# Performance work log

Hardware: AMD Instinct MI355X
Metric: run time of the kernel (lower is better)

## Reference

```python
import jax, jax.numpy as jnp
import numpy as np

B, S, D, F, E = 4, 2048, 1024, 4096, 8


def setup_inputs() -> dict:
    key = jax.random.key(0)
    ks = jax.random.split(key, 7)
    s1 = 1.0 / np.sqrt(D)
    s2 = 1.0 / np.sqrt(F)
    x = jax.random.normal(ks[0], (B, S, D), dtype=jnp.float32)
    # Stacked expert weights: linear1 (D->F), linear2 (F->D), torch default uniform init
    W1 = jax.random.uniform(ks[1], (E, D, F), jnp.float32, -s1, s1)
    b1 = jax.random.uniform(ks[2], (E, F), jnp.float32, -s1, s1)
    W2 = jax.random.uniform(ks[3], (E, F, D), jnp.float32, -s2, s2)
    b2 = jax.random.uniform(ks[4], (E, D), jnp.float32, -s2, s2)
    Wr = jax.random.uniform(ks[5], (D, E), jnp.float32, -s1, s1)
    br = jax.random.uniform(ks[6], (E,), jnp.float32, -s1, s1)
    return {"x": x, "W1": W1, "b1": b1, "W2": W2, "b2": b2, "Wr": Wr, "br": br}


def reference(x, W1, b1, W2, b2, Wr, br):
    b, s, d = x.shape
    e = Wr.shape[1]
    logits = x @ Wr + br                      # [B,S,E]
    idx = jnp.argmax(logits, axis=-1)         # top-1 expert per token
    probs = jax.nn.softmax(logits, axis=-1)
    gates = jnp.take_along_axis(probs, idx[..., None], axis=-1)[..., 0]  # [B,S]
    xf = x.reshape(-1, d)                     # [N,D]
    idxf = idx.reshape(-1)
    gf = gates.reshape(-1)
    out = jnp.zeros_like(xf)
    for ei in range(e):                       # fixed small expert count
        h = jax.nn.gelu(xf @ W1[ei] + b1[ei], approximate=False)  # exact gelu like F.gelu
        y = h @ W2[ei] + b2[ei]
        mask = (idxf == ei).astype(xf.dtype)
        out = out + y * (gf * mask)[:, None]
    return out.reshape(b, s, d)
```

## Files before the change

kernel.cpp:

```cpp
#include <hip/hip_runtime.h>
#include <stdint.h>
#include <math.h>

#define NTOK 8192
#define DIM  1024
#define FDIM 4096
#define NEXP 8

typedef __bf16 bf16x8 __attribute__((ext_vector_type(8)));
typedef float floatx4 __attribute__((ext_vector_type(4)));
typedef unsigned int u32;

__device__ __forceinline__ unsigned short f2b(float f) {
  union { float f; unsigned u; } v; v.f = f;
  return (unsigned short)((v.u + 0x7fffu + ((v.u >> 16) & 1u)) >> 16);
}

__device__ __forceinline__ float gelu_f(float x) {
  float u = 1.5957691216f * x * (1.0f + 0.044715f * x * x);
  return x / (1.0f + __expf(-u));
}

__device__ __forceinline__ void async_cp16(const unsigned short* g, unsigned short* l) {
  __builtin_amdgcn_global_load_lds((__attribute__((address_space(1))) u32*)g,
                                   (__attribute__((address_space(3))) u32*)l, 16, 0, 0);
}

__global__ __launch_bounds__(256) void router_k(
    const float* __restrict__ x, const float* __restrict__ Wr,
    const float* __restrict__ br, int* __restrict__ idx,
    float* __restrict__ gate, int* __restrict__ ctrl) {
  int t = (int)((blockIdx.x * 256 + threadIdx.x) >> 6);
  int lane = threadIdx.x & 63;
  const float* xr = x + (size_t)t * DIM;
  float acc[NEXP];
#pragma unroll
  for (int e = 0; e < NEXP; e++) acc[e] = 0.f;
#pragma unroll
  for (int k = 0; k < DIM / 64; k++) {
    int d = k * 64 + lane;
    float xv = xr[d];
    const float4* wp = (const float4*)(Wr + (size_t)d * NEXP);
    float4 w0 = wp[0], w1 = wp[1];
    acc[0] += xv * w0.x; acc[1] += xv * w0.y;
    acc[2] += xv * w0.z; acc[3] += xv * w0.w;
    acc[4] += xv * w1.x; acc[5] += xv * w1.y;
    acc[6] += xv * w1.z; acc[7] += xv * w1.w;
  }
#pragma unroll
  for (int off = 32; off > 0; off >>= 1) {
#pragma unroll
    for (int e = 0; e < NEXP; e++) acc[e] += __shfl_xor(acc[e], off, 64);
  }
  if (lane == 0) {
    float mx = -3.4e38f; int best = 0;
#pragma unroll
    for (int e = 0; e < NEXP; e++) {
      float l = acc[e] + br[e];
      if (l > mx) { mx = l; best = e; }
    }
    float s = 0.f;
#pragma unroll
    for (int e = 0; e < NEXP; e++) s += expf(acc[e] + br[e] - mx);
    idx[t] = best;
    gate[t] = 1.f / s;
    atomicAdd(&ctrl[best], 1);
  }
}

__global__ void scan_k(int* __restrict__ ctrl) {
  int off = 0, ts = 0;
  ctrl[8] = 0; ctrl[25] = 0;
  for (int e = 0; e < NEXP; e++) {
    off += ctrl[e];                 ctrl[9 + e]  = off;
    ts  += (ctrl[e] + 127) >> 7;    ctrl[26 + e] = ts;
  }
}

__global__ __launch_bounds__(256) void scatter_k(
    const float* __restrict__ x, const int* __restrict__ idx,
    const float* __restrict__ gate, int* __restrict__ ctrl,
    unsigned short* __restrict__ Xb, int* __restrict__ token_dst,
    float* __restrict__ gate_p) {
  __shared__ int s_pos;
  int t = blockIdx.x;
  if (threadIdx.x == 0) {
    int e = idx[t];
    s_pos = ctrl[8 + e] + atomicAdd(&ctrl[17 + e], 1);
  }
  __syncthreads();
  int pos = s_pos;
  if (threadIdx.x == 0) { token_dst[pos] = t; gate_p[pos] = gate[t]; }
  float4 v = ((const float4*)(x + (size_t)t * DIM))[threadIdx.x];
  ushort4 o;
  o.x = f2b(v.x); o.y = f2b(v.y); o.z = f2b(v.z); o.w = f2b(v.w);
  ((ushort4*)(Xb + (size_t)pos * DIM))[threadIdx.x] = o;
}

__global__ __launch_bounds__(256) void transpose_cvt_k(
    const float* __restrict__ in, unsigned short* __restrict__ out,
    int R, int C) {
  __shared__ float tile[64][65];
  __shared__ unsigned short obuf[64][72];
  size_t base = (size_t)blockIdx.z * (size_t)R * (size_t)C;
  int c0 = blockIdx.x * 64, r0 = blockIdx.y * 64;
  int t = threadIdx.x;
  int rr = t >> 4, cc = (t & 15) * 4;
#pragma unroll
  for (int k = 0; k < 64; k += 16) {
    float4 v = *(const float4*)&in[base + (size_t)(r0 + rr + k) * C + c0 + cc];
    tile[rr + k][cc] = v.x; tile[rr + k][cc + 1] = v.y;
    tile[rr + k][cc + 2] = v.z; tile[rr + k][cc + 3] = v.w;
  }
  __syncthreads();
  int cr = t >> 4, rb = (t & 15) * 4;
#pragma unroll
  for (int k = 0; k < 64; k += 16) {
    ushort4 o;
    o.x = f2b(tile[rb + 0][cr + k]); o.y = f2b(tile[rb + 1][cr + k]);
    o.z = f2b(tile[rb + 2][cr + k]); o.w = f2b(tile[rb + 3][cr + k]);
    *(ushort4*)&obuf[cr + k][rb] = o;
  }
  __syncthreads();
  int r2 = t >> 3, c8 = (t & 7) * 8;
#pragma unroll
  for (int k = 0; k < 64; k += 32)
    *(uint4*)&out[base + (size_t)(c0 + r2 + k) * R + r0 + c8] = *(const uint4*)&obuf[r2 + k][c8];
}

__global__ __launch_bounds__(256) void gemm1_k(
    const unsigned short* __restrict__ Amat, const unsigned short* __restrict__ Bmat,
    const float* __restrict__ bias, unsigned short* __restrict__ Hout,
    const int* __restrict__ ctrl) {
  __shared__ unsigned short lds[16384];
  unsigned short* A_lds = lds;
  unsigned short* B_lds = lds + 8192;

  int mt = blockIdx.y;
  if (mt >= ctrl[33]) return;
  int e = 0;
  while (e < 7 && ctrl[26 + e] <= mt) e++;
  int mt_local = mt - ctrl[25 + e];
  int m0 = ctrl[8 + e] + mt_local * 128;
  int cnt = ctrl[e] - mt_local * 128; if (cnt > 128) cnt = 128;
  int c0 = blockIdx.x * 128;
  const unsigned short* B = Bmat + (size_t)e * FDIM * DIM;

  int tid = threadIdx.x;
  int lane = tid & 63, wave = tid >> 6;
  int wr = wave >> 1, wc = wave & 1;
  int grp = lane >> 4, m16 = lane & 15;

  int lr = lane >> 3;
  int cchunk = (lane & 7) ^ lr;
  const unsigned short* srcA[4];
  const unsigned short* srcB[4];
  unsigned short* dstA[4];
  unsigned short* dstB[4];
#pragma unroll
  for (int q = 0; q < 4; q++) {
    int brow = wave * 32 + q * 8;
    int arow = m0 + brow + lr; if (arow > NTOK - 1) arow = NTOK - 1;
    srcA[q] = Amat + (size_t)arow * DIM + cchunk * 8;
    srcB[q] = B + (size_t)(c0 + brow + lr) * DIM + cchunk * 8;
    dstA[q] = A_lds + brow * 64;
    dstB[q] = B_lds + brow * 64;
  }

  floatx4 acc[4][4];
  floatx4 zero = {0.f, 0.f, 0.f, 0.f};
#pragma unroll
  for (int i = 0; i < 4; i++)
#pragma unroll
    for (int j = 0; j < 4; j++) acc[i][j] = zero;

  int x7 = m16 & 7;
  int rowA[4], rowB[4];
#pragma unroll
  for (int i = 0; i < 4; i++) {
    rowA[i] = (wr * 64 + i * 16 + m16) * 64;
    rowB[i] = (wc * 64 + i * 16 + m16) * 64;
  }

  for (int kk = 0; kk < DIM; kk += 64) {
#pragma unroll
    for (int q = 0; q < 4; q++) async_cp16(srcA[q], dstA[q]);
#pragma unroll
    for (int q = 0; q < 4; q++) async_cp16(srcB[q], dstB[q]);
#pragma unroll
    for (int q = 0; q < 4; q++) { srcA[q] += 64; srcB[q] += 64; }
    __syncthreads();
    bf16x8 af[2][4], bfr[2][4];
#pragma unroll
    for (int h = 0; h < 2; h++) {
      int off = (((h << 2) | grp) ^ x7) << 3;
#pragma unroll
      for (int i = 0; i < 4; i++) {
        af[h][i]  = *(const bf16x8*)&A_lds[rowA[i] + off];
        bfr[h][i] = *(const bf16x8*)&B_lds[rowB[i] + off];
      }
    }
#pragma unroll
    for (int h = 0; h < 2; h++)
#pragma unroll
      for (int i = 0; i < 4; i++)
#pragma unroll
        for (int j = 0; j < 4; j++)
          acc[i][j] = __builtin_amdgcn_mfma_f32_16x16x32_bf16(af[h][i], bfr[h][j], acc[i][j], 0, 0, 0);
    __syncthreads();
  }

  float bs[4];
#pragma unroll
  for (int j = 0; j < 4; j++) bs[j] = bias[(size_t)e * FDIM + c0 + wc * 64 + j * 16 + m16];

  unsigned short* st = lds + wave * 4096;
#pragma unroll
  for (int i = 0; i < 4; i++)
#pragma unroll
    for (int j = 0; j < 4; j++)
#pragma unroll
      for (int r = 0; r < 4; r++)
        st[(i * 16 + grp * 4 + r) * 64 + j * 16 + m16] = f2b(gelu_f(acc[i][j][r] + bs[j]));
  __syncthreads();
  int lr8 = lane >> 3, c8 = (lane & 7) * 8;
  int colb = c0 + wc * 64 + c8;
#pragma unroll
  for (int rr = 0; rr < 8; rr++) {
    int row = rr * 8 + lr8;
    int gm = wr * 64 + row;
    if (gm < cnt)
      *(uint4*)&Hout[(size_t)(m0 + gm) * FDIM + colb] = *(const uint4*)&st[row * 64 + c8];
  }
}

__global__ __launch_bounds__(256) void gemm2_k(
    const unsigned short* __restrict__ Hmat, const unsigned short* __restrict__ W2b,
    float* __restrict__ P, const int* __restrict__ ctrl) {
  __shared__ unsigned short lds[16384];
  unsigned short* A_lds = lds;
  unsigned short* B_lds = lds + 8192;

  int mt = blockIdx.y;
  if (mt >= ctrl[33]) return;
  int e = 0;
  while (e < 7 && ctrl[26 + e] <= mt) e++;
  int mt_local = mt - ctrl[25 + e];
  int m0 = ctrl[8 + e] + mt_local * 128;
  int cnt = ctrl[e] - mt_local * 128; if (cnt > 128) cnt = 128;
  int c0 = blockIdx.x * 128;
  int chunk = blockIdx.z;
  int k0 = chunk * (FDIM / 2);
  const unsigned short* B = W2b + (size_t)e * DIM * FDIM + k0;
  const unsigned short* A = Hmat + k0;
  float* Pc = P + (size_t)chunk * NTOK * DIM;

  int tid = threadIdx.x;
  int lane = tid & 63, wave = tid >> 6;
  int wr = wave >> 1, wc = wave & 1;
  int grp = lane >> 4, m16 = lane & 15;

  int lr = lane >> 3;
  int cchunk = (lane & 7) ^ lr;
  const unsigned short* srcA[4];
  const unsigned short* srcB[4];
  unsigned short* dstA[4];
  unsigned short* dstB[4];
#pragma unroll
  for (int q = 0; q < 4; q++) {
    int brow = wave * 32 + q * 8;
    int arow = m0 + brow + lr; if (arow > NTOK - 1) arow = NTOK - 1;
    srcA[q] = A + (size_t)arow * FDIM + cchunk * 8;
    srcB[q] = B + (size_t)(c0 + brow + lr) * FDIM + cchunk * 8;
    dstA[q] = A_lds + brow * 64;
    dstB[q] = B_lds + brow * 64;
  }

  floatx4 acc[4][4];
  floatx4 zero = {0.f, 0.f, 0.f, 0.f};
#pragma unroll
  for (int i = 0; i < 4; i++)
#pragma unroll
    for (int j = 0; j < 4; j++) acc[i][j] = zero;

  int x7 = m16 & 7;
  int rowA[4], rowB[4];
#pragma unroll
  for (int i = 0; i < 4; i++) {
    rowA[i] = (wr * 64 + i * 16 + m16) * 64;
    rowB[i] = (wc * 64 + i * 16 + m16) * 64;
  }

  for (int kk = 0; kk < FDIM / 2; kk += 64) {
#pragma unroll
    for (int q = 0; q < 4; q++) async_cp16(srcA[q], dstA[q]);
#pragma unroll
    for (int q = 0; q < 4; q++) async_cp16(srcB[q], dstB[q]);
#pragma unroll
    for (int q = 0; q < 4; q++) { srcA[q] += 64; srcB[q] += 64; }
    __syncthreads();
    bf16x8 af[2][4], bfr[2][4];
#pragma unroll
    for (int h = 0; h < 2; h++) {
      int off = (((h << 2) | grp) ^ x7) << 3;
#pragma unroll
      for (int i = 0; i < 4; i++) {
        af[h][i]  = *(const bf16x8*)&A_lds[rowA[i] + off];
        bfr[h][i] = *(const bf16x8*)&B_lds[rowB[i] + off];
      }
    }
#pragma unroll
    for (int h = 0; h < 2; h++)
#pragma unroll
      for (int i = 0; i < 4; i++)
#pragma unroll
        for (int j = 0; j < 4; j++)
          acc[i][j] = __builtin_amdgcn_mfma_f32_16x16x32_bf16(af[h][i], bfr[h][j], acc[i][j], 0, 0, 0);
    __syncthreads();
  }

#pragma unroll
  for (int i = 0; i < 4; i++) {
    int rb = wr * 64 + i * 16 + grp * 4;
#pragma unroll
    for (int r = 0; r < 4; r++) {
      int lm = rb + r;
      if (lm < cnt) {
#pragma unroll
        for (int j = 0; j < 4; j++) {
          int col = c0 + wc * 64 + j * 16 + m16;
          Pc[(size_t)(m0 + lm) * DIM + col] = acc[i][j][r];
        }
      }
    }
  }
}

__global__ __launch_bounds__(256) void reduce_k(
    const float* __restrict__ P, const float* __restrict__ b2,
    float* __restrict__ out, const int* __restrict__ token_dst,
    const float* __restrict__ gate_p, const int* __restrict__ ctrl) {
  int row = blockIdx.x;
  int e = 0;
  while (e < 7 && ctrl[9 + e] <= row) e++;
  int t = token_dst[row];
  float g = gate_p[row];
  int c = threadIdx.x * 4;
  float4 p0 = *(const float4*)&P[(size_t)row * DIM + c];
  float4 p1 = *(const float4*)&P[(size_t)(NTOK + row) * DIM + c];
  float4 bb = *(const float4*)&b2[(size_t)e * DIM + c];
  float4 o;
  o.x = (p0.x + p1.x + bb.x) * g;
  o.y = (p0.y + p1.y + bb.y) * g;
  o.z = (p0.z + p1.z + bb.z) * g;
  o.w = (p0.w + p1.w + bb.w) * g;
  *(float4*)&out[(size_t)t * DIM + c] = o;
}

extern "C" void kernel_launch(void* const* d_in, const int* in_sizes, int n_in,
                              void* d_out, int out_size, void* d_ws, size_t ws_size,
                              hipStream_t stream) {
  const float* x  = (const float*)d_in[0];
  const float* W1 = (const float*)d_in[1];
  const float* b1 = (const float*)d_in[2];
  const float* W2 = (const float*)d_in[3];
  const float* b2 = (const float*)d_in[4];
  const float* Wr = (const float*)d_in[5];
  const float* br = (const float*)d_in[6];
  float* out = (float*)d_out;

  char* w = (char*)d_ws;
  int*   ctrl      = (int*)w;
  int*   idx       = (int*)(w + 1024);
  float* gate      = (float*)(w + 1024 + 4 * NTOK);
  int*   token_dst = (int*)(w + 1024 + 8 * NTOK);
  float* gate_p    = (float*)(w + 1024 + 12 * NTOK);
  unsigned short* Xb  = (unsigned short*)(w + (1ull << 18));
  unsigned short* H   = (unsigned short*)(w + (20ull << 20));
  unsigned short* W1b = (unsigned short*)(w + (88ull << 20));
  unsigned short* W2b = (unsigned short*)(w + (156ull << 20));
  float*          P   = (float*)(w + (88ull << 20));

  hipMemsetAsync(ctrl, 0, 256, stream);
  router_k<<<NTOK / 4, 256, 0, stream>>>(x, Wr, br, idx, gate, ctrl);
  scan_k<<<1, 1, 0, stream>>>(ctrl);
  scatter_k<<<NTOK, 256, 0, stream>>>(x, idx, gate, ctrl, Xb, token_dst, gate_p);
  transpose_cvt_k<<<dim3(FDIM / 64, DIM / 64, NEXP), 256, 0, stream>>>(W1, W1b, DIM, FDIM);
  transpose_cvt_k<<<dim3(DIM / 64, FDIM / 64, NEXP), 256, 0, stream>>>(W2, W2b, FDIM, DIM);
  gemm1_k<<<dim3(FDIM / 128, 72), 256, 0, stream>>>(Xb, W1b, b1, H, ctrl);
  gemm2_k<<<dim3(DIM / 128, 72, 2), 256, 0, stream>>>(H, W2b, P, ctrl);
  reduce_k<<<NTOK, 256, 0, stream>>>(P, b2, out, token_dst, gate_p, ctrl);
}
```

Before: 792.1 us.

## Fuse bias/gate epilogue into gemm2, drop split-K, merge weight transposes, pad LDS

Removes the split-K partial buffer and the separate reduce kernel: gemm2 now runs the full K range and applies the bias and gate, scattering results directly to output rows. The two weight transpose/convert launches are merged into a single launch. The gemm1 epilogue staging buffer gets a padded row stride to reduce LDS bank conflicts. The trade-off is that gemm2 has half as many blocks, each with a K loop twice as long, which lowers parallelism, and its output stores are scattered by token.

```diff
diff --git a/kernel.cpp b/kernel.cpp
--- a/kernel.cpp
+++ b/kernel.cpp
@@ -97,18 +97,27 @@
   ((ushort4*)(Xb + (size_t)pos * DIM))[threadIdx.x] = o;
 }
 
-__global__ __launch_bounds__(256) void transpose_cvt_k(
-    const float* __restrict__ in, unsigned short* __restrict__ out,
-    int R, int C) {
+__global__ __launch_bounds__(256) void transpose_cvt2_k(
+    const float* __restrict__ W1, unsigned short* __restrict__ W1b,
+    const float* __restrict__ W2, unsigned short* __restrict__ W2b) {
   __shared__ float tile[64][65];
   __shared__ unsigned short obuf[64][72];
-  size_t base = (size_t)blockIdx.z * (size_t)R * (size_t)C;
-  int c0 = blockIdx.x * 64, r0 = blockIdx.y * 64;
+  int z = blockIdx.z;
+  const float* in; unsigned short* out; int R, C, tc, tr;
+  if (z < NEXP) {
+    in = W1 + (size_t)z * DIM * FDIM; out = W1b + (size_t)z * DIM * FDIM;
+    R = DIM; C = FDIM; tc = blockIdx.x; tr = blockIdx.y;
+  } else {
+    int e = z - NEXP;
+    in = W2 + (size_t)e * FDIM * DIM; out = W2b + (size_t)e * FDIM * DIM;
+    R = FDIM; C = DIM; tc = blockIdx.y; tr = blockIdx.x;
+  }
+  int c0 = tc * 64, r0 = tr * 64;
   int t = threadIdx.x;
   int rr = t >> 4, cc = (t & 15) * 4;
 #pragma unroll
   for (int k = 0; k < 64; k += 16) {
-    float4 v = *(const float4*)&in[base + (size_t)(r0 + rr + k) * C + c0 + cc];
+    float4 v = *(const float4*)&in[(size_t)(r0 + rr + k) * C + c0 + cc];
     tile[rr + k][cc] = v.x; tile[rr + k][cc + 1] = v.y;
     tile[rr + k][cc + 2] = v.z; tile[rr + k][cc + 3] = v.w;
   }
@@ -125,14 +134,14 @@
   int r2 = t >> 3, c8 = (t & 7) * 8;
 #pragma unroll
   for (int k = 0; k < 64; k += 32)
-    *(uint4*)&out[base + (size_t)(c0 + r2 + k) * R + r0 + c8] = *(const uint4*)&obuf[r2 + k][c8];
+    *(uint4*)&out[(size_t)(c0 + r2 + k) * R + r0 + c8] = *(const uint4*)&obuf[r2 + k][c8];
 }
 
 __global__ __launch_bounds__(256) void gemm1_k(
     const unsigned short* __restrict__ Amat, const unsigned short* __restrict__ Bmat,
     const float* __restrict__ bias, unsigned short* __restrict__ Hout,
     const int* __restrict__ ctrl) {
-  __shared__ unsigned short lds[16384];
+  __shared__ unsigned short lds[17408];
   unsigned short* A_lds = lds;
   unsigned short* B_lds = lds + 8192;
 
@@ -214,14 +223,14 @@
 #pragma unroll
   for (int j = 0; j < 4; j++) bs[j] = bias[(size_t)e * FDIM + c0 + wc * 64 + j * 16 + m16];
 
-  unsigned short* st = lds + wave * 4096;
+  unsigned short* st = lds + wave * 4352;
 #pragma unroll
   for (int i = 0; i < 4; i++)
 #pragma unroll
     for (int j = 0; j < 4; j++)
 #pragma unroll
       for (int r = 0; r < 4; r++)
-        st[(i * 16 + grp * 4 + r) * 64 + j * 16 + m16] = f2b(gelu_f(acc[i][j][r] + bs[j]));
+        st[(i * 16 + grp * 4 + r) * 68 + j * 16 + m16] = f2b(gelu_f(acc[i][j][r] + bs[j]));
   __syncthreads();
   int lr8 = lane >> 3, c8 = (lane & 7) * 8;
   int colb = c0 + wc * 64 + c8;
@@ -229,14 +238,20 @@
   for (int rr = 0; rr < 8; rr++) {
     int row = rr * 8 + lr8;
     int gm = wr * 64 + row;
-    if (gm < cnt)
-      *(uint4*)&Hout[(size_t)(m0 + gm) * FDIM + colb] = *(const uint4*)&st[row * 64 + c8];
+    if (gm < cnt) {
+      uint2 a = *(const uint2*)&st[row * 68 + c8];
+      uint2 b = *(const uint2*)&st[row * 68 + c8 + 4];
+      uint4 v; v.x = a.x; v.y = a.y; v.z = b.x; v.w = b.y;
+      *(uint4*)&Hout[(size_t)(m0 + gm) * FDIM + colb] = v;
+    }
   }
 }
 
 __global__ __launch_bounds__(256) void gemm2_k(
     const unsigned short* __restrict__ Hmat, const unsigned short* __restrict__ W2b,
-    float* __restrict__ P, const int* __restrict__ ctrl) {
+    const float* __restrict__ b2, float* __restrict__ out,
+    const int* __restrict__ token_dst, const float* __restrict__ gate_p,
+    const int* __restrict__ ctrl) {
   __shared__ unsigned short lds[16384];
   unsigned short* A_lds = lds;
   unsigned short* B_lds = lds + 8192;
@@ -249,11 +264,7 @@
   int m0 = ctrl[8 + e] + mt_local * 128;
   int cnt = ctrl[e] - mt_local * 128; if (cnt > 128) cnt = 128;
   int c0 = blockIdx.x * 128;
-  int chunk = blockIdx.z;
-  int k0 = chunk * (FDIM / 2);
-  const unsigned short* B = W2b + (size_t)e * DIM * FDIM + k0;
-  const unsigned short* A = Hmat + k0;
-  float* Pc = P + (size_t)chunk * NTOK * DIM;
+  const unsigned short* B = W2b + (size_t)e * DIM * FDIM;
 
   int tid = threadIdx.x;
   int lane = tid & 63, wave = tid >> 6;
@@ -270,7 +281,7 @@
   for (int q = 0; q < 4; q++) {
     int brow = wave * 32 + q * 8;
     int arow = m0 + brow + lr; if (arow > NTOK - 1) arow = NTOK - 1;
-    srcA[q] = A + (size_t)arow * FDIM + cchunk * 8;
+    srcA[q] = Hmat + (size_t)arow * FDIM + cchunk * 8;
     srcB[q] = B + (size_t)(c0 + brow + lr) * FDIM + cchunk * 8;
     dstA[q] = A_lds + brow * 64;
     dstB[q] = B_lds + brow * 64;
@@ -291,7 +302,7 @@
     rowB[i] = (wc * 64 + i * 16 + m16) * 64;
   }
 
-  for (int kk = 0; kk < FDIM / 2; kk += 64) {
+  for (int kk = 0; kk < FDIM; kk += 64) {
 #pragma unroll
     for (int q = 0; q < 4; q++) async_cp16(srcA[q], dstA[q]);
 #pragma unroll
@@ -319,6 +330,10 @@
     __syncthreads();
   }
 
+  float bs[4];
+#pragma unroll
+  for (int j = 0; j < 4; j++) bs[j] = b2[(size_t)e * DIM + c0 + wc * 64 + j * 16 + m16];
+
 #pragma unroll
   for (int i = 0; i < 4; i++) {
     int rb = wr * 64 + i * 16 + grp * 4;
@@ -326,35 +341,16 @@
     for (int r = 0; r < 4; r++) {
       int lm = rb + r;
       if (lm < cnt) {
+        int t = token_dst[m0 + lm];
+        float g = gate_p[m0 + lm];
 #pragma unroll
         for (int j = 0; j < 4; j++) {
           int col = c0 + wc * 64 + j * 16 + m16;
-          Pc[(size_t)(m0 + lm) * DIM + col] = acc[i][j][r];
+          out[(size_t)t * DIM + col] = (acc[i][j][r] + bs[j]) * g;
         }
       }
     }
   }
-}
-
-__global__ __launch_bounds__(256) void reduce_k(
-    const float* __restrict__ P, const float* __restrict__ b2,
-    float* __restrict__ out, const int* __restrict__ token_dst,
-    const float* __restrict__ gate_p, const int* __restrict__ ctrl) {
-  int row = blockIdx.x;
-  int e = 0;
-  while (e < 7 && ctrl[9 + e] <= row) e++;
-  int t = token_dst[row];
-  float g = gate_p[row];
-  int c = threadIdx.x * 4;
-  float4 p0 = *(const float4*)&P[(size_t)row * DIM + c];
-  float4 p1 = *(const float4*)&P[(size_t)(NTOK + row) * DIM + c];
-  float4 bb = *(const float4*)&b2[(size_t)e * DIM + c];
-  float4 o;
-  o.x = (p0.x + p1.x + bb.x) * g;
-  o.y = (p0.y + p1.y + bb.y) * g;
-  o.z = (p0.z + p1.z + bb.z) * g;
-  o.w = (p0.w + p1.w + bb.w) * g;
-  *(float4*)&out[(size_t)t * DIM + c] = o;
 }
 
 extern "C" void kernel_launch(void* const* d_in, const int* in_sizes, int n_in,
@@ -379,15 +375,12 @@
   unsigned short* H   = (unsigned short*)(w + (20ull << 20));
   unsigned short* W1b = (unsigned short*)(w + (88ull << 20));
   unsigned short* W2b = (unsigned short*)(w + (156ull << 20));
-  float*          P   = (float*)(w + (88ull << 20));
 
   hipMemsetAsync(ctrl, 0, 256, stream);
   router_k<<<NTOK / 4, 256, 0, stream>>>(x, Wr, br, idx, gate, ctrl);
   scan_k<<<1, 1, 0, stream>>>(ctrl);
   scatter_k<<<NTOK, 256, 0, stream>>>(x, idx, gate, ctrl, Xb, token_dst, gate_p);
-  transpose_cvt_k<<<dim3(FDIM / 64, DIM / 64, NEXP), 256, 0, stream>>>(W1, W1b, DIM, FDIM);
-  transpose_cvt_k<<<dim3(DIM / 64, FDIM / 64, NEXP), 256, 0, stream>>>(W2, W2b, FDIM, DIM);
+  transpose_cvt2_k<<<dim3(64, 16, 16), 256, 0, stream>>>(W1, W1b, W2, W2b);
   gemm1_k<<<dim3(FDIM / 128, 72), 256, 0, stream>>>(Xb, W1b, b1, H, ctrl);
-  gemm2_k<<<dim3(DIM / 128, 72, 2), 256, 0, stream>>>(H, W2b, P, ctrl);
-  reduce_k<<<NTOK, 256, 0, stream>>>(P, b2, out, token_dst, gate_p, ctrl);
-}
+  gemm2_k<<<dim3(DIM / 128, 72), 256, 0, stream>>>(H, W2b, b2, out, token_dst, gate_p, ctrl);
+}
```

Measured after the change: 807.5 us. About the same (+1.9%).
